# Kernel tuning notes

Hardware: AMD Instinct MI355X
Metric: run time of the kernel (lower is better)

## Reference

```python
import jax, jax.numpy as jnp
import numpy as np

EPS = 1e-5


def gcn_conv(x, edge_index, W, b):
    # PyG GCNConv: h = x @ W; add self-loops; symmetric deg^-1/2 normalization; scatter-add to dst; + bias
    n = x.shape[0]
    h = x @ W  # [N, out]
    loops = jnp.arange(n, dtype=edge_index.dtype)
    src = jnp.concatenate([edge_index[0], loops])
    dst = jnp.concatenate([edge_index[1], loops])
    deg = jax.ops.segment_sum(jnp.ones(src.shape[0], dtype=h.dtype), dst, num_segments=n)
    dinv = jnp.where(deg > 0, jax.lax.rsqrt(jnp.maximum(deg, 1e-12)), 0.0)
    norm = dinv[src] * dinv[dst]  # [E+N]
    out = jax.ops.segment_sum(h[src] * norm[:, None], dst, num_segments=n)
    return out + b


def setup_inputs() -> dict:
    key = jax.random.key(0)
    ks = jax.random.split(key, 10)
    N, E = 50000, 800000
    IN, HID, OUT = 128, 128, 64
    x = jax.random.normal(ks[0], (N, IN), dtype=jnp.float32)
    edge_index1 = jax.random.randint(ks[1], (2, E), 0, N, dtype=jnp.int64)
    edge_index2 = jax.random.randint(ks[2], (2, E), 0, N, dtype=jnp.int64)
    s1 = 1.0 / np.sqrt(IN)
    s2 = 1.0 / np.sqrt(HID)
    W1 = jax.random.uniform(ks[3], (IN, HID), jnp.float32, -s1, s1)
    b1 = jax.random.uniform(ks[4], (HID,), jnp.float32, -s1, s1)
    gamma = jnp.ones((HID,), jnp.float32)
    beta = jnp.zeros((HID,), jnp.float32)
    W2 = jax.random.uniform(ks[5], (HID, OUT), jnp.float32, -s2, s2)
    b2 = jax.random.uniform(ks[6], (OUT,), jnp.float32, -s2, s2)
    return {"x": x, "edge_index1": edge_index1, "edge_index2": edge_index2,
            "W1": W1, "b1": b1, "gamma": gamma, "beta": beta, "W2": W2, "b2": b2}


def reference(x, edge_index1, edge_index2, W1, b1, gamma, beta, W2, b2):
    # layer 1: GCNConv -> (save hidden) -> BatchNorm1d (batch stats) -> ReLU -> dropout (identity, deterministic)
    h = gcn_conv(x, edge_index1, W1, b1)
    hidden = h
    mean = jnp.mean(h, axis=0)
    var = jnp.mean((h - mean) ** 2, axis=0)  # biased var, as torch BN uses for normalization
    h = (h - mean) * jax.lax.rsqrt(var + EPS) * gamma + beta
    h = jax.nn.relu(h)
    # layer 2: GCNConv (no norm/act on last layer)
    out = gcn_conv(h, edge_index2, W2, b2)
    return (out, hidden)
```

## Files before the change

kernel.cpp:

```cpp
#include <hip/hip_runtime.h>

#define GN 50000
#define GE 800000
#define HID 128
#define OUTC 64
#define NBK 196
#define NW  196
#define EPW 4096
#define PCAP 5888
#define A1B 2048

#define OFF_H1    0
#define OFF_H2    3200000
#define OFF_DINV1 4800000
#define OFF_DINV2 4850000
#define OFF_ROW1  4900000
#define OFF_ROW2  4950004
#define OFF_HIST  5000008
#define OFF_TOT   5076840
#define OFF_BBASE 5077232
#define OFF_BN    5077632
#define OFF_PART  5078144
#define OFF_PARTA 5602432
#define OFF_SRC1  5606528
#define OFF_SRC2  6406528

__device__ inline unsigned bf16rne(float f) {
  unsigned u = __float_as_uint(f);
  return (u + 0x7FFFu + ((u >> 16) & 1u)) >> 16;
}
__device__ inline unsigned pack2(float a, float b) {
  return bf16rne(a) | (bf16rne(b) << 16);
}
__device__ inline float bflo(unsigned w) { return __uint_as_float(w << 16); }
__device__ inline float bfhi(unsigned w) { return __uint_as_float(w & 0xFFFF0000u); }
__device__ inline float bfs(unsigned short w) { return __uint_as_float(((unsigned)w) << 16); }

__global__ __launch_bounds__(256) void p1hist_kernel(const int* __restrict__ e1,
    const int* __restrict__ e2, int* __restrict__ hist) {
  __shared__ int h[NBK];
  int g = blockIdx.y, w = blockIdx.x;
  const int* dst = (g ? e2 : e1) + GE;
  for (int i = threadIdx.x; i < NBK; i += 256) h[i] = 0;
  __syncthreads();
  int i0 = w * EPW, iend = i0 + EPW; if (iend > GE) iend = GE;
  for (int i = i0 + threadIdx.x; i < iend; i += 256)
    atomicAdd(&h[dst[i] >> 8], 1);
  __syncthreads();
  int* out = hist + ((size_t)g * NW + w) * NBK;
  for (int i = threadIdx.x; i < NBK; i += 256) out[i] = h[i];
}

__global__ __launch_bounds__(256) void histscanA_kernel(int* __restrict__ hist,
    int* __restrict__ tot) {
  __shared__ int lds[256];
  int b = blockIdx.x, g = blockIdx.y, t = threadIdx.x;
  int* col = hist + (size_t)g * NW * NBK + b;
  int v = (t < NW) ? col[(size_t)t * NBK] : 0;
  lds[t] = v;
  __syncthreads();
  for (int off = 1; off < 256; off <<= 1) {
    int u = (t >= off) ? lds[t - off] : 0;
    __syncthreads();
    lds[t] += u;
    __syncthreads();
  }
  if (t < NW) col[(size_t)t * NBK] = lds[t] - v;
  if (t == NW - 1) tot[g * NBK + b] = lds[t];
}

__global__ __launch_bounds__(256) void histscanB_kernel(const int* __restrict__ tot,
    int* __restrict__ bbase) {
  __shared__ int lds[256];
  int t = threadIdx.x;
  for (int g = 0; g < 2; ++g) {
    int v = (t < NBK) ? tot[g * NBK + t] : 0;
    int orig = v;
    lds[t] = v;
    __syncthreads();
    for (int off = 1; off < 256; off <<= 1) {
      int u = (t >= off) ? lds[t - off] : 0;
      __syncthreads();
      lds[t] += u;
      __syncthreads();
    }
    if (t < NBK) bbase[g * (NBK + 1) + t] = lds[t] - orig;
    if (t == NBK - 1) bbase[g * (NBK + 1) + NBK] = lds[t];
    __syncthreads();
  }
}

__global__ __launch_bounds__(256) void p1scat_kernel(const int* __restrict__ e1,
    const int* __restrict__ e2, const int* __restrict__ hist,
    const int* __restrict__ bbase, int* __restrict__ pb1, int* __restrict__ pb2) {
  __shared__ int off[NBK];
  int g = blockIdx.y, w = blockIdx.x;
  const int* e = g ? e2 : e1;
  int* pb = g ? pb2 : pb1;
  const int* hrow = hist + ((size_t)g * NW + w) * NBK;
  const int* bb = bbase + g * (NBK + 1);
  for (int i = threadIdx.x; i < NBK; i += 256) off[i] = bb[i] + hrow[i];
  __syncthreads();
  int i0 = w * EPW, iend = i0 + EPW; if (iend > GE) iend = GE;
  for (int i = i0 + threadIdx.x; i < iend; i += 256) {
    int d = e[GE + i], s = e[i];
    int p = atomicAdd(&off[d >> 8], 1);
    pb[p] = s | ((d & 255) << 16);
  }
}

__global__ __launch_bounds__(256) void p2sort_kernel(const int* __restrict__ pb1,
    const int* __restrict__ pb2, const int* __restrict__ bbase,
    int* __restrict__ row1, int* __restrict__ row2,
    float* __restrict__ dinv1, float* __restrict__ dinv2,
    int* __restrict__ src1, int* __restrict__ src2) {
  __shared__ int stage[PCAP];
  __shared__ int lcnt[256], lc2[256], arr[256];
  __shared__ int lrow[257];
  int g = blockIdx.y, b = blockIdx.x, t = threadIdx.x;
  const int* pb = g ? pb2 : pb1;
  const int* bb = bbase + g * (NBK + 1);
  int* row = g ? row2 : row1;
  float* dinv = g ? dinv2 : dinv1;
  int* src = g ? src2 : src1;
  int lo = b << 8, hi = lo + 256; if (hi > GN) hi = GN;
  int nn = hi - lo;
  int base = bb[b], end = bb[b + 1], L = end - base;
  lcnt[t] = 0; lc2[t] = 0;
  __syncthreads();
  for (int i = base + t; i < end; i += 256)
    atomicAdd(&lcnt[((unsigned)pb[i]) >> 16], 1);
  __syncthreads();
  int v = lcnt[t];
  arr[t] = v;
  __syncthreads();
  for (int off = 1; off < 256; off <<= 1) {
    int u = (t >= off) ? arr[t - off] : 0;
    __syncthreads();
    arr[t] += u;
    __syncthreads();
  }
  lrow[t] = arr[t] - v;
  if (t == 255) lrow[256] = arr[255];
  __syncthreads();
  if (t < nn) {
    row[lo + t] = base + lrow[t];
    dinv[lo + t] = rsqrtf(1.0f + (float)lcnt[t]);
  }
  if (b == NBK - 1 && t == 0) row[GN] = end;
  if (L <= PCAP) {
    for (int i = base + t; i < end; i += 256) {
      unsigned p = (unsigned)pb[i];
      int ld = p >> 16;
      int rk = atomicAdd(&lc2[ld], 1);
      stage[lrow[ld] + rk] = (int)(p & 0xFFFFu);
    }
    __syncthreads();
    for (int i = t; i < L; i += 256) src[base + i] = stage[i];
  } else {
    for (int i = base + t; i < end; i += 256) {
      unsigned p = (unsigned)pb[i];
      int ld = p >> 16;
      int rk = atomicAdd(&lc2[ld], 1);
      src[base + lrow[ld] + rk] = (int)(p & 0xFFFFu);
    }
  }
}

__global__ __launch_bounds__(256) void gemm1_kernel(const float* __restrict__ A,
    const float* __restrict__ B, const float* __restrict__ dinv1,
    unsigned* __restrict__ h1b) {
  __shared__ __align__(16) float wlds[128 * 64];
  __shared__ __align__(16) float alds[32 * 128];
  int t = threadIdx.x;
  int row0 = blockIdx.x * 32;
  int cb = blockIdx.y * 64;
  for (int i = t; i < 128 * 16; i += 256) {
    int k = i >> 4, c4 = i & 15;
    ((float4*)wlds)[i] = ((const float4*)B)[k * 32 + (cb >> 2) + c4];
  }
  for (int i = t; i < 1024; i += 256) {
    int r = i >> 5, c4 = i & 31;
    int gr = row0 + r;
    ((float4*)alds)[i] = (gr < GN) ? ((const float4*)A)[(size_t)gr * 32 + c4]
                                   : make_float4(0.f, 0.f, 0.f, 0.f);
  }
  __syncthreads();
  int j0 = (t & 15) * 4;
  int r0 = (t >> 4) * 2;
  float4 acc0 = {0, 0, 0, 0}, acc1 = {0, 0, 0, 0};
  #pragma unroll 8
  for (int k = 0; k < 128; ++k) {
    float4 w = *(const float4*)&wlds[k * 64 + j0];
    float a0 = alds[r0 * 128 + k];
    float a1 = alds[(r0 + 1) * 128 + k];
    acc0.x += a0 * w.x; acc0.y += a0 * w.y; acc0.z += a0 * w.z; acc0.w += a0 * w.w;
    acc1.x += a1 * w.x; acc1.y += a1 * w.y; acc1.z += a1 * w.z; acc1.w += a1 * w.w;
  }
  int gr0 = row0 + r0;
  if (gr0 < GN) {
    float dv = dinv1[gr0];
    uint2 p = make_uint2(pack2(dv * acc0.x, dv * acc0.y), pack2(dv * acc0.z, dv * acc0.w));
    ((uint2*)h1b)[((size_t)gr0 * 128 + cb + j0) >> 2] = p;
  }
  if (gr0 + 1 < GN) {
    float dv = dinv1[gr0 + 1];
    uint2 p = make_uint2(pack2(dv * acc1.x, dv * acc1.y), pack2(dv * acc1.z, dv * acc1.w));
    ((uint2*)h1b)[((size_t)(gr0 + 1) * 128 + cb + j0) >> 2] = p;
  }
}

__global__ __launch_bounds__(256) void gemm2_kernel(const float* __restrict__ A,
    const float* __restrict__ B, const float* __restrict__ scale,
    const float* __restrict__ shift, const float* __restrict__ dinv2,
    unsigned* __restrict__ h2b) {
  __shared__ __align__(16) float wlds[128 * 64];
  __shared__ __align__(16) float alds[32 * 128];
  __shared__ float sc[128], sh[128];
  int t = threadIdx.x;
  if (t < 128) { sc[t] = scale[t]; sh[t] = shift[t]; }
  int row0 = blockIdx.x * 32;
  for (int i = t; i < 128 * 16; i += 256)
    ((float4*)wlds)[i] = ((const float4*)B)[i];
  __syncthreads();
  for (int i = t; i < 1024; i += 256) {
    int r = i >> 5, c4 = i & 31;
    int gr = row0 + r;
    float4 v = (gr < GN) ? ((const float4*)A)[(size_t)gr * 32 + c4]
                         : make_float4(0.f, 0.f, 0.f, 0.f);
    int c = c4 * 4;
    v.x = fmaxf(fmaf(v.x, sc[c],     sh[c]),     0.f);
    v.y = fmaxf(fmaf(v.y, sc[c + 1], sh[c + 1]), 0.f);
    v.z = fmaxf(fmaf(v.z, sc[c + 2], sh[c + 2]), 0.f);
    v.w = fmaxf(fmaf(v.w, sc[c + 3], sh[c + 3]), 0.f);
    ((float4*)alds)[i] = v;
  }
  __syncthreads();
  int j0 = (t & 15) * 4;
  int r0 = (t >> 4) * 2;
  float4 acc0 = {0, 0, 0, 0}, acc1 = {0, 0, 0, 0};
  #pragma unroll 8
  for (int k = 0; k < 128; ++k) {
    float4 w = *(const float4*)&wlds[k * 64 + j0];
    float a0 = alds[r0 * 128 + k];
    float a1 = alds[(r0 + 1) * 128 + k];
    acc0.x += a0 * w.x; acc0.y += a0 * w.y; acc0.z += a0 * w.z; acc0.w += a0 * w.w;
    acc1.x += a1 * w.x; acc1.y += a1 * w.y; acc1.z += a1 * w.z; acc1.w += a1 * w.w;
  }
  int gr0 = row0 + r0;
  if (gr0 < GN) {
    float dv = dinv2[gr0];
    uint2 p = make_uint2(pack2(dv * acc0.x, dv * acc0.y), pack2(dv * acc0.z, dv * acc0.w));
    ((uint2*)h2b)[((size_t)gr0 * 64 + j0) >> 2] = p;
  }
  if (gr0 + 1 < GN) {
    float dv = dinv2[gr0 + 1];
    uint2 p = make_uint2(pack2(dv * acc1.x, dv * acc1.y), pack2(dv * acc1.z, dv * acc1.w));
    ((uint2*)h2b)[((size_t)(gr0 + 1) * 64 + j0) >> 2] = p;
  }
}

__global__ __launch_bounds__(256) void agg1_kernel(const unsigned* __restrict__ h1b,
    const int* __restrict__ row, const int* __restrict__ srcs,
    const float* __restrict__ dinv, const float* __restrict__ b1,
    float* __restrict__ hidden, float* __restrict__ part) {
  __shared__ float ps[256];
  int t = threadIdx.x;
  int lane = t & 63;
  float2 b = ((const float2*)b1)[lane];
  float sx = 0.f, sy = 0.f, qx = 0.f, qy = 0.f;
  int wid = (blockIdx.x * 256 + t) >> 6;
  for (int d = wid; d < GN; d += A1B * 4) {
    float di = dinv[d];
    unsigned sw = h1b[(size_t)d * 64 + lane];
    float ax = bflo(sw), ay = bfhi(sw);
    int e0 = row[d], e1 = row[d + 1];
    int i = e0;
    while ((i & 3) && i < e1) {
      unsigned v = h1b[(size_t)srcs[i] * 64 + lane];
      ax += bflo(v); ay += bfhi(v);
      ++i;
    }
    for (; i + 8 <= e1; i += 8) {
      int4 sa = *(const int4*)&srcs[i];
      int4 sb = *(const int4*)&srcs[i + 4];
      unsigned v0 = h1b[(size_t)sa.x * 64 + lane], v1 = h1b[(size_t)sa.y * 64 + lane];
      unsigned v2 = h1b[(size_t)sa.z * 64 + lane], v3 = h1b[(size_t)sa.w * 64 + lane];
      unsigned v4 = h1b[(size_t)sb.x * 64 + lane], v5 = h1b[(size_t)sb.y * 64 + lane];
      unsigned v6 = h1b[(size_t)sb.z * 64 + lane], v7 = h1b[(size_t)sb.w * 64 + lane];
      ax += bflo(v0); ay += bfhi(v0);
      ax += bflo(v1); ay += bfhi(v1);
      ax += bflo(v2); ay += bfhi(v2);
      ax += bflo(v3); ay += bfhi(v3);
      ax += bflo(v4); ay += bfhi(v4);
      ax += bflo(v5); ay += bfhi(v5);
      ax += bflo(v6); ay += bfhi(v6);
      ax += bflo(v7); ay += bfhi(v7);
    }
    if (i + 4 <= e1) {
      int4 sa = *(const int4*)&srcs[i];
      unsigned v0 = h1b[(size_t)sa.x * 64 + lane], v1 = h1b[(size_t)sa.y * 64 + lane];
      unsigned v2 = h1b[(size_t)sa.z * 64 + lane], v3 = h1b[(size_t)sa.w * 64 + lane];
      ax += bflo(v0); ay += bfhi(v0);
      ax += bflo(v1); ay += bfhi(v1);
      ax += bflo(v2); ay += bfhi(v2);
      ax += bflo(v3); ay += bfhi(v3);
      i += 4;
    }
    for (; i < e1; ++i) {
      unsigned v = h1b[(size_t)srcs[i] * 64 + lane];
      ax += bflo(v); ay += bfhi(v);
    }
    float ox = ax * di + b.x, oy = ay * di + b.y;
    float2 o; o.x = ox; o.y = oy;
    ((float2*)(hidden + (size_t)d * 128))[lane] = o;
    sx += ox; sy += oy; qx += ox * ox; qy += oy * oy;
  }
  float* pout = part + (size_t)blockIdx.x * 256;
  ps[t] = sx; __syncthreads();
  if (t < 64) pout[2 * t] = ps[t] + ps[t + 64] + ps[t + 128] + ps[t + 192];
  __syncthreads();
  ps[t] = sy; __syncthreads();
  if (t < 64) pout[2 * t + 1] = ps[t] + ps[t + 64] + ps[t + 128] + ps[t + 192];
  __syncthreads();
  ps[t] = qx; __syncthreads();
  if (t < 64) pout[128 + 2 * t] = ps[t] + ps[t + 64] + ps[t + 128] + ps[t + 192];
  __syncthreads();
  ps[t] = qy; __syncthreads();
  if (t < 64) pout[128 + 2 * t + 1] = ps[t] + ps[t + 64] + ps[t + 128] + ps[t + 192];
}

__global__ __launch_bounds__(256) void bn_reduceA_kernel(const float* __restrict__ part,
    float* __restrict__ partA) {
  int r = blockIdx.x, t = threadIdx.x;
  float s = 0.f;
  for (int k = 0; k < A1B / 16; ++k)
    s += part[((size_t)r * (A1B / 16) + k) * 256 + t];
  partA[r * 256 + t] = s;
}

__global__ __launch_bounds__(128) void bn_final_kernel(const float* __restrict__ partA,
    const float* __restrict__ gamma, const float* __restrict__ beta,
    float* __restrict__ scale, float* __restrict__ shift) {
  int c = threadIdx.x;
  float S = 0.f, Q = 0.f;
  for (int r = 0; r < 16; ++r) {
    S += partA[r * 256 + c];
    Q += partA[r * 256 + 128 + c];
  }
  float mean = S * (1.0f / GN);
  float var = Q * (1.0f / GN) - mean * mean;
  float istd = rsqrtf(var + 1e-5f);
  float g = gamma[c] * istd;
  scale[c] = g;
  shift[c] = beta[c] - mean * g;
}

__global__ __launch_bounds__(256) void agg2_kernel(const unsigned short* __restrict__ h2b,
    const int* __restrict__ row, const int* __restrict__ srcs,
    const float* __restrict__ dinv, const float* __restrict__ b2,
    float* __restrict__ out) {
  int wave = (blockIdx.x * 256 + threadIdx.x) >> 6;
  int lane = threadIdx.x & 63;
  if (wave >= GN) return;
  int d = wave;
  float di = dinv[d];
  float acc = bfs(h2b[(size_t)d * 64 + lane]);
  int e0 = row[d], e1 = row[d + 1];
  int i = e0;
  while ((i & 3) && i < e1) {
    acc += bfs(h2b[(size_t)srcs[i] * 64 + lane]);
    ++i;
  }
  for (; i + 8 <= e1; i += 8) {
    int4 sa = *(const int4*)&srcs[i];
    int4 sb = *(const int4*)&srcs[i + 4];
    float v0 = bfs(h2b[(size_t)sa.x * 64 + lane]), v1 = bfs(h2b[(size_t)sa.y * 64 + lane]);
    float v2 = bfs(h2b[(size_t)sa.z * 64 + lane]), v3 = bfs(h2b[(size_t)sa.w * 64 + lane]);
    float v4 = bfs(h2b[(size_t)sb.x * 64 + lane]), v5 = bfs(h2b[(size_t)sb.y * 64 + lane]);
    float v6 = bfs(h2b[(size_t)sb.z * 64 + lane]), v7 = bfs(h2b[(size_t)sb.w * 64 + lane]);
    acc += v0 + v1 + v2 + v3 + v4 + v5 + v6 + v7;
  }
  if (i + 4 <= e1) {
    int4 sa = *(const int4*)&srcs[i];
    acc += bfs(h2b[(size_t)sa.x * 64 + lane]) + bfs(h2b[(size_t)sa.y * 64 + lane])
         + bfs(h2b[(size_t)sa.z * 64 + lane]) + bfs(h2b[(size_t)sa.w * 64 + lane]);
    i += 4;
  }
  for (; i < e1; ++i)
    acc += bfs(h2b[(size_t)srcs[i] * 64 + lane]);
  out[(size_t)d * 64 + lane] = acc * di + b2[lane];
}

extern "C" void kernel_launch(void* const* d_in, const int* in_sizes, int n_in,
                              void* d_out, int out_size, void* d_ws, size_t ws_size,
                              hipStream_t stream) {
  const float* x     = (const float*)d_in[0];
  const int*   e1    = (const int*)d_in[1];
  const int*   e2    = (const int*)d_in[2];
  const float* W1    = (const float*)d_in[3];
  const float* b1    = (const float*)d_in[4];
  const float* gamma = (const float*)d_in[5];
  const float* beta  = (const float*)d_in[6];
  const float* W2    = (const float*)d_in[7];
  const float* b2    = (const float*)d_in[8];

  float* out    = (float*)d_out;
  float* hidden = out + (size_t)GN * OUTC;

  float*          ws    = (float*)d_ws;
  unsigned*       h1b   = (unsigned*)(ws + OFF_H1);
  unsigned*       h2b   = (unsigned*)(ws + OFF_H2);
  float*          dinv1 = ws + OFF_DINV1;
  float*          dinv2 = ws + OFF_DINV2;
  int*            row1  = (int*)(ws + OFF_ROW1);
  int*            row2  = (int*)(ws + OFF_ROW2);
  int*            hist  = (int*)(ws + OFF_HIST);
  int*            tot   = (int*)(ws + OFF_TOT);
  int*            bbase = (int*)(ws + OFF_BBASE);
  float*          bnbuf = ws + OFF_BN;
  float*          part  = ws + OFF_PART;
  float*          partA = ws + OFF_PARTA;
  int*            src1  = (int*)(ws + OFF_SRC1);
  int*            src2  = (int*)(ws + OFF_SRC2);
  int*            pb1   = (int*)h2b;
  int*            pb2   = pb1 + GE;

  p1hist_kernel<<<dim3(NW, 2), 256, 0, stream>>>(e1, e2, hist);
  histscanA_kernel<<<dim3(NBK, 2), 256, 0, stream>>>(hist, tot);
  histscanB_kernel<<<1, 256, 0, stream>>>(tot, bbase);
  p1scat_kernel<<<dim3(NW, 2), 256, 0, stream>>>(e1, e2, hist, bbase, pb1, pb2);
  p2sort_kernel<<<dim3(NBK, 2), 256, 0, stream>>>(pb1, pb2, bbase,
                                                  row1, row2, dinv1, dinv2, src1, src2);

  gemm1_kernel<<<dim3((GN + 31) / 32, 2), 256, 0, stream>>>(x, W1, dinv1, h1b);
  agg1_kernel<<<A1B, 256, 0, stream>>>(h1b, row1, src1, dinv1, b1, hidden, part);

  bn_reduceA_kernel<<<16, 256, 0, stream>>>(part, partA);
  bn_final_kernel<<<1, 128, 0, stream>>>(partA, gamma, beta, bnbuf, bnbuf + 128);

  gemm2_kernel<<<dim3((GN + 31) / 32, 1), 256, 0, stream>>>(hidden, W2,
                                                            bnbuf, bnbuf + 128, dinv2, h2b);
  agg2_kernel<<<(GN * 64 + 255) / 256, 256, 0, stream>>>(
      (const unsigned short*)h2b, row2, src2, dinv2, b2, out);
}
```

Measured before the change: 275.9 us.

## Use bf16 MFMA for both dense GEMMs with pre-transposed bf16 weights

Replaces the scalar FP32 FMA GEMMs with bf16 MFMA 16x16x32 instructions. A new kernel converts W1/W2 into transposed, pair-packed bf16 layouts. Activations are packed to bf16 in padded LDS tiles, and each block now covers 64 rows and all output columns, so x is read once instead of twice. This adds bf16 rounding of the GEMM inputs and uses scalar 2-byte output stores, which may be less coalesced than the old vector stores.

```diff
diff --git a/kernel.cpp b/kernel.cpp
--- a/kernel.cpp
+++ b/kernel.cpp
@@ -24,6 +24,11 @@
 #define OFF_PARTA 5602432
 #define OFF_SRC1  5606528
 #define OFF_SRC2  6406528
+#define OFF_WT1   7206528
+#define OFF_WT2   7214720
+
+typedef __attribute__((ext_vector_type(8))) short bf16x8;
+typedef __attribute__((ext_vector_type(4))) float f32x4;
 
 __device__ inline unsigned bf16rne(float f) {
   unsigned u = __float_as_uint(f);
@@ -167,96 +172,128 @@
   }
 }
 
+__global__ __launch_bounds__(256) void wcvt_kernel(const float* __restrict__ W1,
+    const float* __restrict__ W2, unsigned* __restrict__ wt1, unsigned* __restrict__ wt2) {
+  int t = blockIdx.x * 256 + threadIdx.x;
+  if (t < 8192) {
+    int n = t >> 6, k2 = t & 63;
+    wt1[t] = pack2(W1[(2 * k2) * 128 + n], W1[(2 * k2 + 1) * 128 + n]);
+  }
+  if (t < 4096) {
+    int n = t >> 6, k2 = t & 63;
+    wt2[t] = pack2(W2[(2 * k2) * 64 + n], W2[(2 * k2 + 1) * 64 + n]);
+  }
+}
+
 __global__ __launch_bounds__(256) void gemm1_kernel(const float* __restrict__ A,
-    const float* __restrict__ B, const float* __restrict__ dinv1,
-    unsigned* __restrict__ h1b) {
-  __shared__ __align__(16) float wlds[128 * 64];
-  __shared__ __align__(16) float alds[32 * 128];
+    const unsigned* __restrict__ wt1, const float* __restrict__ dinv1,
+    unsigned short* __restrict__ h1u) {
+  __shared__ unsigned a_lds[64 * 68];
+  __shared__ unsigned w_lds[128 * 68];
   int t = threadIdx.x;
-  int row0 = blockIdx.x * 32;
-  int cb = blockIdx.y * 64;
-  for (int i = t; i < 128 * 16; i += 256) {
-    int k = i >> 4, c4 = i & 15;
-    ((float4*)wlds)[i] = ((const float4*)B)[k * 32 + (cb >> 2) + c4];
-  }
-  for (int i = t; i < 1024; i += 256) {
-    int r = i >> 5, c4 = i & 31;
-    int gr = row0 + r;
-    ((float4*)alds)[i] = (gr < GN) ? ((const float4*)A)[(size_t)gr * 32 + c4]
-                                   : make_float4(0.f, 0.f, 0.f, 0.f);
-  }
-  __syncthreads();
-  int j0 = (t & 15) * 4;
-  int r0 = (t >> 4) * 2;
-  float4 acc0 = {0, 0, 0, 0}, acc1 = {0, 0, 0, 0};
-  #pragma unroll 8
-  for (int k = 0; k < 128; ++k) {
-    float4 w = *(const float4*)&wlds[k * 64 + j0];
-    float a0 = alds[r0 * 128 + k];
-    float a1 = alds[(r0 + 1) * 128 + k];
-    acc0.x += a0 * w.x; acc0.y += a0 * w.y; acc0.z += a0 * w.z; acc0.w += a0 * w.w;
-    acc1.x += a1 * w.x; acc1.y += a1 * w.y; acc1.z += a1 * w.z; acc1.w += a1 * w.w;
-  }
-  int gr0 = row0 + r0;
-  if (gr0 < GN) {
-    float dv = dinv1[gr0];
-    uint2 p = make_uint2(pack2(dv * acc0.x, dv * acc0.y), pack2(dv * acc0.z, dv * acc0.w));
-    ((uint2*)h1b)[((size_t)gr0 * 128 + cb + j0) >> 2] = p;
-  }
-  if (gr0 + 1 < GN) {
-    float dv = dinv1[gr0 + 1];
-    uint2 p = make_uint2(pack2(dv * acc1.x, dv * acc1.y), pack2(dv * acc1.z, dv * acc1.w));
-    ((uint2*)h1b)[((size_t)(gr0 + 1) * 128 + cb + j0) >> 2] = p;
+  int row0 = blockIdx.x * 64;
+  for (int i = t; i < 128 * 64; i += 256)
+    w_lds[(i >> 6) * 68 + (i & 63)] = wt1[i];
+  for (int i = t; i < 64 * 32; i += 256) {
+    int m = i >> 5, k4 = i & 31;
+    int gr = row0 + m;
+    float4 v = (gr < GN) ? ((const float4*)A)[(size_t)gr * 32 + k4]
+                         : make_float4(0.f, 0.f, 0.f, 0.f);
+    unsigned* dst = &a_lds[m * 68 + k4 * 2];
+    dst[0] = pack2(v.x, v.y);
+    dst[1] = pack2(v.z, v.w);
+  }
+  __syncthreads();
+  int lane = t & 63, w = t >> 6;
+  int n16 = lane & 15, quad = lane >> 4;
+  int mbase = (w & 1) * 32;
+  int nbase = (w >> 1) * 64;
+  f32x4 acc[2][4] = {};
+  const unsigned short* als = (const unsigned short*)a_lds;
+  const unsigned short* wls = (const unsigned short*)w_lds;
+  #pragma unroll
+  for (int ks = 0; ks < 4; ++ks) {
+    int k0 = ks * 32 + quad * 8;
+    bf16x8 a0 = *(const bf16x8*)(als + (mbase + n16) * 136 + k0);
+    bf16x8 a1 = *(const bf16x8*)(als + (mbase + 16 + n16) * 136 + k0);
+    #pragma unroll
+    for (int nt = 0; nt < 4; ++nt) {
+      bf16x8 bf = *(const bf16x8*)(wls + (nbase + nt * 16 + n16) * 136 + k0);
+      acc[0][nt] = __builtin_amdgcn_mfma_f32_16x16x32_bf16(a0, bf, acc[0][nt], 0, 0, 0);
+      acc[1][nt] = __builtin_amdgcn_mfma_f32_16x16x32_bf16(a1, bf, acc[1][nt], 0, 0, 0);
+    }
+  }
+  #pragma unroll
+  for (int mt = 0; mt < 2; ++mt) {
+    #pragma unroll
+    for (int r = 0; r < 4; ++r) {
+      int row_g = row0 + mbase + mt * 16 + quad * 4 + r;
+      if (row_g < GN) {
+        float dv = dinv1[row_g];
+        #pragma unroll
+        for (int nt = 0; nt < 4; ++nt) {
+          int col = nbase + nt * 16 + n16;
+          h1u[(size_t)row_g * 128 + col] = (unsigned short)bf16rne(dv * acc[mt][nt][r]);
+        }
+      }
+    }
   }
 }
 
 __global__ __launch_bounds__(256) void gemm2_kernel(const float* __restrict__ A,
-    const float* __restrict__ B, const float* __restrict__ scale,
+    const unsigned* __restrict__ wt2, const float* __restrict__ scale,
     const float* __restrict__ shift, const float* __restrict__ dinv2,
-    unsigned* __restrict__ h2b) {
-  __shared__ __align__(16) float wlds[128 * 64];
-  __shared__ __align__(16) float alds[32 * 128];
+    unsigned short* __restrict__ h2u) {
+  __shared__ unsigned a_lds[64 * 68];
+  __shared__ unsigned w_lds[64 * 68];
   __shared__ float sc[128], sh[128];
   int t = threadIdx.x;
   if (t < 128) { sc[t] = scale[t]; sh[t] = shift[t]; }
-  int row0 = blockIdx.x * 32;
-  for (int i = t; i < 128 * 16; i += 256)
-    ((float4*)wlds)[i] = ((const float4*)B)[i];
-  __syncthreads();
-  for (int i = t; i < 1024; i += 256) {
-    int r = i >> 5, c4 = i & 31;
-    int gr = row0 + r;
-    float4 v = (gr < GN) ? ((const float4*)A)[(size_t)gr * 32 + c4]
+  int row0 = blockIdx.x * 64;
+  for (int i = t; i < 64 * 64; i += 256)
+    w_lds[(i >> 6) * 68 + (i & 63)] = wt2[i];
+  __syncthreads();
+  for (int i = t; i < 64 * 32; i += 256) {
+    int m = i >> 5, k4 = i & 31;
+    int gr = row0 + m;
+    float4 v = (gr < GN) ? ((const float4*)A)[(size_t)gr * 32 + k4]
                          : make_float4(0.f, 0.f, 0.f, 0.f);
-    int c = c4 * 4;
+    int c = k4 * 4;
     v.x = fmaxf(fmaf(v.x, sc[c],     sh[c]),     0.f);
     v.y = fmaxf(fmaf(v.y, sc[c + 1], sh[c + 1]), 0.f);
     v.z = fmaxf(fmaf(v.z, sc[c + 2], sh[c + 2]), 0.f);
     v.w = fmaxf(fmaf(v.w, sc[c + 3], sh[c + 3]), 0.f);
-    ((float4*)alds)[i] = v;
-  }
-  __syncthreads();
-  int j0 = (t & 15) * 4;
-  int r0 = (t >> 4) * 2;
-  float4 acc0 = {0, 0, 0, 0}, acc1 = {0, 0, 0, 0};
-  #pragma unroll 8
-  for (int k = 0; k < 128; ++k) {
-    float4 w = *(const float4*)&wlds[k * 64 + j0];
-    float a0 = alds[r0 * 128 + k];
-    float a1 = alds[(r0 + 1) * 128 + k];
-    acc0.x += a0 * w.x; acc0.y += a0 * w.y; acc0.z += a0 * w.z; acc0.w += a0 * w.w;
-    acc1.x += a1 * w.x; acc1.y += a1 * w.y; acc1.z += a1 * w.z; acc1.w += a1 * w.w;
-  }
-  int gr0 = row0 + r0;
-  if (gr0 < GN) {
-    float dv = dinv2[gr0];
-    uint2 p = make_uint2(pack2(dv * acc0.x, dv * acc0.y), pack2(dv * acc0.z, dv * acc0.w));
-    ((uint2*)h2b)[((size_t)gr0 * 64 + j0) >> 2] = p;
-  }
-  if (gr0 + 1 < GN) {
-    float dv = dinv2[gr0 + 1];
-    uint2 p = make_uint2(pack2(dv * acc1.x, dv * acc1.y), pack2(dv * acc1.z, dv * acc1.w));
-    ((uint2*)h2b)[((size_t)(gr0 + 1) * 64 + j0) >> 2] = p;
+    unsigned* dst = &a_lds[m * 68 + k4 * 2];
+    dst[0] = pack2(v.x, v.y);
+    dst[1] = pack2(v.z, v.w);
+  }
+  __syncthreads();
+  int lane = t & 63, w = t >> 6;
+  int n16 = lane & 15, quad = lane >> 4;
+  f32x4 acc[4] = {};
+  const unsigned short* als = (const unsigned short*)a_lds;
+  const unsigned short* wls = (const unsigned short*)w_lds;
+  #pragma unroll
+  for (int ks = 0; ks < 4; ++ks) {
+    int k0 = ks * 32 + quad * 8;
+    bf16x8 af = *(const bf16x8*)(als + (w * 16 + n16) * 136 + k0);
+    #pragma unroll
+    for (int nt = 0; nt < 4; ++nt) {
+      bf16x8 bf = *(const bf16x8*)(wls + (nt * 16 + n16) * 136 + k0);
+      acc[nt] = __builtin_amdgcn_mfma_f32_16x16x32_bf16(af, bf, acc[nt], 0, 0, 0);
+    }
+  }
+  #pragma unroll
+  for (int r = 0; r < 4; ++r) {
+    int row_g = row0 + w * 16 + quad * 4 + r;
+    if (row_g < GN) {
+      float dv = dinv2[row_g];
+      #pragma unroll
+      for (int nt = 0; nt < 4; ++nt) {
+        int col = nt * 16 + n16;
+        h2u[(size_t)row_g * 64 + col] = (unsigned short)bf16rne(dv * acc[nt][r]);
+      }
+    }
   }
 }
 
@@ -423,9 +460,12 @@
   float*          partA = ws + OFF_PARTA;
   int*            src1  = (int*)(ws + OFF_SRC1);
   int*            src2  = (int*)(ws + OFF_SRC2);
+  unsigned*       wt1   = (unsigned*)(ws + OFF_WT1);
+  unsigned*       wt2   = (unsigned*)(ws + OFF_WT2);
   int*            pb1   = (int*)h2b;
   int*            pb2   = pb1 + GE;
 
+  wcvt_kernel<<<32, 256, 0, stream>>>(W1, W2, wt1, wt2);
   p1hist_kernel<<<dim3(NW, 2), 256, 0, stream>>>(e1, e2, hist);
   histscanA_kernel<<<dim3(NBK, 2), 256, 0, stream>>>(hist, tot);
   histscanB_kernel<<<1, 256, 0, stream>>>(tot, bbase);
@@ -433,14 +473,15 @@
   p2sort_kernel<<<dim3(NBK, 2), 256, 0, stream>>>(pb1, pb2, bbase,
                                                   row1, row2, dinv1, dinv2, src1, src2);
 
-  gemm1_kernel<<<dim3((GN + 31) / 32, 2), 256, 0, stream>>>(x, W1, dinv1, h1b);
+  gemm1_kernel<<<(GN + 63) / 64, 256, 0, stream>>>(x, wt1, dinv1,
+                                                   (unsigned short*)h1b);
   agg1_kernel<<<A1B, 256, 0, stream>>>(h1b, row1, src1, dinv1, b1, hidden, part);
 
   bn_reduceA_kernel<<<16, 256, 0, stream>>>(part, partA);
   bn_final_kernel<<<1, 128, 0, stream>>>(partA, gamma, beta, bnbuf, bnbuf + 128);
 
-  gemm2_kernel<<<dim3((GN + 31) / 32, 1), 256, 0, stream>>>(hidden, W2,
-                                                            bnbuf, bnbuf + 128, dinv2, h2b);
+  gemm2_kernel<<<(GN + 63) / 64, 256, 0, stream>>>(hidden, wt2, bnbuf, bnbuf + 128,
+                                                   dinv2, (unsigned short*)h2b);
   agg2_kernel<<<(GN * 64 + 255) / 256, 256, 0, stream>>>(
       (const unsigned short*)h2b, row2, src2, dinv2, b2, out);
 }
```

Result: faster. 230.4 us (-16.5%).
